# Kernel optimization log

Measured on AMD Instinct MI355X. Metric: run time of the kernel, lower is better.

## Reference

```python
import jax, jax.numpy as jnp
import numpy as np

BATCH = 8192
IN_F = 4096
OUT_F = 4096


def setup_inputs() -> dict:
    key = jax.random.key(0)
    k_x, k_w, k_m = jax.random.split(key, 3)
    x = jax.random.normal(k_x, (BATCH, IN_F), dtype=jnp.float32)
    # kaiming_normal_ for relu: std = sqrt(2 / fan_in) with fan_in = in_features
    std = float(np.sqrt(2.0 / IN_F))
    weight = jax.random.normal(k_w, (OUT_F, IN_F), dtype=jnp.float32) * std
    bias = jnp.zeros((OUT_F,), dtype=jnp.float32)
    mask = jax.random.bernoulli(k_m, 0.5, (OUT_F, IN_F)).astype(jnp.float32)
    return {"x": x, "weight": weight, "bias": bias, "mask": mask}


def reference(x, weight, bias, mask):
    # masked_weight = weight * mask; out = x @ masked_weight.T + bias
    masked_weight = weight * mask                      # [out, in]
    return jnp.einsum("bi,oi->bo", x, masked_weight) + bias  # [batch, out]
```

## Files before the change

kernel.cpp:

```cpp
#include <hip/hip_runtime.h>
#include <stdint.h>

#define BATCH 8192
#define IN_F  4096
#define OUT_F 4096

#define BM 256
#define BN 256
#define BK 64
#define KT (IN_F / BK)

typedef __attribute__((ext_vector_type(8))) short bf16x8;
typedef __attribute__((ext_vector_type(4))) float f32x4;


__device__ __forceinline__ unsigned short f2bf(float f) {
    unsigned int u = __float_as_uint(f);
    unsigned int lsb = (u >> 16) & 1u;
    u += 0x7fffu + lsb;
    return (unsigned short)(u >> 16);
}

__device__ __forceinline__ void gl_lds16(const void* g, void* l) {
    __builtin_amdgcn_global_load_lds(
        (const __attribute__((address_space(1))) void*)g,
        (__attribute__((address_space(3))) void*)l,
        16, 0, 0);
}

#define XF4 (BATCH * IN_F / 4)
#define WF4 (OUT_F * IN_F / 4)

__global__ __launch_bounds__(256) void cvt_kernel(const float4* __restrict__ x,
                                                  const float4* __restrict__ w,
                                                  const float4* __restrict__ m,
                                                  uint2* __restrict__ xo,
                                                  uint2* __restrict__ wo) {
    const int i = blockIdx.x * 256 + threadIdx.x;
    union { unsigned short u[4]; uint2 v; } r;
    if (i < XF4) {
        const float4 a = x[i];
        r.u[0] = f2bf(a.x); r.u[1] = f2bf(a.y);
        r.u[2] = f2bf(a.z); r.u[3] = f2bf(a.w);
        xo[i] = r.v;
    } else {
        const int j = i - XF4;
        const float4 a = w[j];
        const float4 b = m[j];
        r.u[0] = f2bf(a.x * b.x); r.u[1] = f2bf(a.y * b.y);
        r.u[2] = f2bf(a.z * b.z); r.u[3] = f2bf(a.w * b.w);
        wo[j] = r.v;
    }
}

__global__ __launch_bounds__(512, 2) void gemm_kernel(const unsigned short* __restrict__ A,
                                                      const unsigned short* __restrict__ W,
                                                      const float* __restrict__ bias,
                                                      float* __restrict__ C) {
    __shared__ __align__(16) char smem[131072];
    char* sA = smem;
    char* sB = smem + 65536;

    const int tid  = threadIdx.x;
    const int lane = tid & 63;
    const int wave = tid >> 6;
    const int wm   = wave >> 2;
    const int wn   = wave & 3;

    const int wg = ((blockIdx.x & 7) << 6) | (blockIdx.x >> 3);
    const int bm = wg >> 4;
    const int bn = wg & 15;

    const int r15 = lane & 15;
    const int g   = lane >> 4;
    const int k0  = (g ^ (r15 & 7)) << 4;

    int ldso[4];
    const unsigned short* gAp[4];
    const unsigned short* gBp[4];
#pragma unroll
    for (int i = 0; i < 4; ++i) {
        const int s   = i * 512 + tid;
        const int row = s >> 3;
        const int ch  = (s & 7) ^ (row & 7);
        ldso[i] = s * 16;
        gAp[i] = A + (size_t)(bm * BM + row) * IN_F + ch * 8;
        gBp[i] = W + (size_t)(bn * BN + row) * IN_F + ch * 8;
    }

#define GLA(buf, ktn, sl) gl_lds16(gAp[sl] + (ktn) * BK, sA + (buf) * 32768 + ldso[sl])
#define GLB(buf, ktn, sl) gl_lds16(gBp[sl] + (ktn) * BK, sB + (buf) * 32768 + ldso[sl])

    f32x4 acc[8][4] = {};
    bf16x8 af[2][2], bgf[4][2];

#define RDA(p)                                                               \
    do {                                                                     \
        _Pragma("unroll")                                                    \
        for (int i = 0; i < 2; ++i)                                          \
            _Pragma("unroll")                                                \
            for (int ks = 0; ks < 2; ++ks)                                   \
                af[i][ks] = *(const bf16x8*)(aB2 + ((p) * 2 + i) * 2048 +    \
                                             (k0 ^ (ks << 6)));              \
    } while (0)
#define RDB()                                                                \
    do {                                                                     \
        _Pragma("unroll")                                                    \
        for (int nf = 0; nf < 4; ++nf)                                       \
            _Pragma("unroll")                                                \
            for (int ks = 0; ks < 2; ++ks)                                   \
                bgf[nf][ks] = *(const bf16x8*)(bB2 + nf * 2048 +             \
                                               (k0 ^ (ks << 6)));            \
    } while (0)
#define MM(p)                                                                \
    do {                                                                     \
        __builtin_amdgcn_s_setprio(1);                                       \
        _Pragma("unroll")                                                    \
        for (int ks = 0; ks < 2; ++ks)                                       \
            _Pragma("unroll")                                                \
            for (int i = 0; i < 2; ++i)                                      \
                _Pragma("unroll")                                            \
                for (int nf = 0; nf < 4; ++nf)                               \
                    acc[(p) * 2 + i][nf] =                                   \
                        __builtin_amdgcn_mfma_f32_16x16x32_bf16(             \
                            af[i][ks], bgf[nf][ks], acc[(p) * 2 + i][nf],    \
                            0, 0, 0);                                        \
        __builtin_amdgcn_s_setprio(0);                                       \
    } while (0)
#define LG0   asm volatile("s_waitcnt lgkmcnt(0)" ::: "memory")
#define SBAR  __builtin_amdgcn_s_barrier()
#define SCH0  __builtin_amdgcn_sched_barrier(0)

    GLB(0, 0, 0); GLB(0, 0, 1); GLB(0, 0, 2); GLB(0, 0, 3);
    GLA(0, 0, 0); GLA(0, 0, 2); GLA(0, 0, 1); GLA(0, 0, 3);
    asm volatile("s_waitcnt vmcnt(2)" ::: "memory");
    SBAR; SCH0;

#pragma unroll 1
    for (int kt = 0; kt < KT; ++kt) {
        const int buf  = kt & 1;
        const int nb   = buf ^ 1;
        const bool more = (kt + 1 < KT);
        const char* aB2 = sA + buf * 32768 + ((wm * 128 + r15) << 7);
        const char* bB2 = sB + buf * 32768 + ((wn * 64 + r15) << 7);

        RDB(); RDA(0);
        if (more) { GLB(nb, kt + 1, 0); GLB(nb, kt + 1, 1); }
        asm volatile("s_waitcnt lgkmcnt(8)" ::: "memory");
        SBAR; LG0; SCH0;
        MM(0);
        SCH0; SBAR; SCH0;

        RDA(1);
        if (more) { GLB(nb, kt + 1, 2); GLB(nb, kt + 1, 3); }
        SBAR; LG0; SCH0;
        MM(1);
        SCH0;
        if (more) { asm volatile("s_waitcnt vmcnt(4)" ::: "memory"); }
        else      { asm volatile("s_waitcnt vmcnt(0)" ::: "memory"); }
        SBAR; SCH0;

        RDA(2);
        if (more) { GLA(nb, kt + 1, 0); GLA(nb, kt + 1, 2); }
        SBAR; LG0; SCH0;
        MM(2);
        SCH0; SBAR; SCH0;

        RDA(3);
        if (more) { GLA(nb, kt + 1, 1); GLA(nb, kt + 1, 3); }
        SBAR; LG0; SCH0;
        MM(3);
        SCH0;
        if (more) { asm volatile("s_waitcnt vmcnt(2)" ::: "memory"); }
        SBAR; SCH0;
    }
#undef GLA
#undef GLB
#undef RDA
#undef RDB
#undef MM
#undef LG0
#undef SBAR
#undef SCH0

    const int crow0 = bm * BM + wm * 128 + g * 4;
    const int ccol0 = bn * BN + wn * 64 + r15;
#pragma unroll
    for (int nf = 0; nf < 4; ++nf) {
        const int col = ccol0 + nf * 16;
        const float bj = bias[col];
#pragma unroll
        for (int mf = 0; mf < 8; ++mf)
#pragma unroll
            for (int reg = 0; reg < 4; ++reg) {
                const int row = crow0 + mf * 16 + reg;
                C[(size_t)row * OUT_F + col] = acc[mf][nf][reg] + bj;
            }
    }
}

__global__ __launch_bounds__(256) void fallback_kernel(const float* __restrict__ x,
                                                       const float* __restrict__ w,
                                                       const float* __restrict__ bias,
                                                       const float* __restrict__ m,
                                                       float* __restrict__ out) {
    size_t idx = (size_t)blockIdx.x * 256 + threadIdx.x;
    int row = (int)(idx >> 12);
    int col = (int)(idx & (OUT_F - 1));
    const float4* xr = (const float4*)(x + (size_t)row * IN_F);
    const float4* wr = (const float4*)(w + (size_t)col * IN_F);
    const float4* mr = (const float4*)(m + (size_t)col * IN_F);
    float s = 0.f;
    for (int k = 0; k < IN_F / 4; ++k) {
        float4 xv = xr[k], wv = wr[k], mv = mr[k];
        s += xv.x * wv.x * mv.x + xv.y * wv.y * mv.y +
             xv.z * wv.z * mv.z + xv.w * wv.w * mv.w;
    }
    out[idx] = s + bias[col];
}


extern "C" void kernel_launch(void* const* d_in, const int* in_sizes, int n_in,
                              void* d_out, int out_size, void* d_ws, size_t ws_size,
                              hipStream_t stream) {
    const float* x    = (const float*)d_in[0];
    const float* w    = (const float*)d_in[1];
    const float* bias = (const float*)d_in[2];
    const float* mask = (const float*)d_in[3];
    float* out = (float*)d_out;

    const size_t need = ((size_t)BATCH * IN_F + (size_t)OUT_F * IN_F) * sizeof(unsigned short);
    if (ws_size < need) {
        fallback_kernel<<<(size_t)BATCH * OUT_F / 256, 256, 0, stream>>>(
            x, w, bias, mask, out);
        return;
    }

    unsigned short* xb = (unsigned short*)d_ws;
    unsigned short* wb = xb + (size_t)BATCH * IN_F;

    cvt_kernel<<<(XF4 + WF4) / 256, 256, 0, stream>>>(
        (const float4*)x, (const float4*)w, (const float4*)mask,
        (uint2*)xb, (uint2*)wb);

    gemm_kernel<<<512, 512, 0, stream>>>(xb, wb, bias, out);
}
```

Measured before the change: 541.2 us.

## Triple-buffer B tiles and register-double-buffer A fragments to cut barriers

```diff
diff --git a/kernel.cpp b/kernel.cpp
--- a/kernel.cpp
+++ b/kernel.cpp
@@ -57,7 +57,7 @@
                                                       const unsigned short* __restrict__ W,
                                                       const float* __restrict__ bias,
                                                       float* __restrict__ C) {
-    __shared__ __align__(16) char smem[131072];
+    __shared__ __align__(16) char smem[163840];
     char* sA = smem;
     char* sB = smem + 65536;
 
@@ -77,7 +77,6 @@
 
     int ldso[4];
     const unsigned short* gAp[4];
-    const unsigned short* gBp[4];
 #pragma unroll
     for (int i = 0; i < 4; ++i) {
         const int s   = i * 512 + tid;
@@ -85,34 +84,37 @@
         const int ch  = (s & 7) ^ (row & 7);
         ldso[i] = s * 16;
         gAp[i] = A + (size_t)(bm * BM + row) * IN_F + ch * 8;
-        gBp[i] = W + (size_t)(bn * BN + row) * IN_F + ch * 8;
-    }
-
-#define GLA(buf, ktn, sl) gl_lds16(gAp[sl] + (ktn) * BK, sA + (buf) * 32768 + ldso[sl])
-#define GLB(buf, ktn, sl) gl_lds16(gBp[sl] + (ktn) * BK, sB + (buf) * 32768 + ldso[sl])
+    }
+    const ptrdiff_t bdel = (W + (size_t)bn * BN * IN_F) - (A + (size_t)bm * BM * IN_F);
+
+#define GLA(aoffb, ktn, sl) gl_lds16(gAp[sl] + (ktn) * BK, sA + (aoffb) + ldso[sl])
+#define GLB(boffb, ktn, sl) gl_lds16(gAp[sl] + bdel + (ktn) * BK, sB + (boffb) + ldso[sl])
+
+    const int arow = (wm * 128 + r15) << 7;
+    const int brow = (wn * 64 + r15) << 7;
 
     f32x4 acc[8][4] = {};
-    bf16x8 af[2][2], bgf[4][2];
-
-#define RDA(p)                                                               \
+    bf16x8 afA[2][2], afB[2][2], bgf[4][2];
+
+#define RDA(q, DST, abase)                                                   \
     do {                                                                     \
         _Pragma("unroll")                                                    \
         for (int i = 0; i < 2; ++i)                                          \
             _Pragma("unroll")                                                \
             for (int ks = 0; ks < 2; ++ks)                                   \
-                af[i][ks] = *(const bf16x8*)(aB2 + ((p) * 2 + i) * 2048 +    \
-                                             (k0 ^ (ks << 6)));              \
+                DST[i][ks] = *(const bf16x8*)((abase) +                      \
+                    (((q) * 32 + i * 16) << 7) + (k0 ^ (ks << 6)));          \
     } while (0)
-#define RDB()                                                                \
+#define RDB(bbase)                                                           \
     do {                                                                     \
         _Pragma("unroll")                                                    \
         for (int nf = 0; nf < 4; ++nf)                                       \
             _Pragma("unroll")                                                \
             for (int ks = 0; ks < 2; ++ks)                                   \
-                bgf[nf][ks] = *(const bf16x8*)(bB2 + nf * 2048 +             \
+                bgf[nf][ks] = *(const bf16x8*)((bbase) + nf * 2048 +         \
                                                (k0 ^ (ks << 6)));            \
     } while (0)
-#define MM(p)                                                                \
+#define MM(p, AX)                                                            \
     do {                                                                     \
         __builtin_amdgcn_s_setprio(1);                                       \
         _Pragma("unroll")                                                    \
@@ -123,63 +125,76 @@
                 for (int nf = 0; nf < 4; ++nf)                               \
                     acc[(p) * 2 + i][nf] =                                   \
                         __builtin_amdgcn_mfma_f32_16x16x32_bf16(             \
-                            af[i][ks], bgf[nf][ks], acc[(p) * 2 + i][nf],    \
+                            AX[i][ks], bgf[nf][ks], acc[(p) * 2 + i][nf],    \
                             0, 0, 0);                                        \
         __builtin_amdgcn_s_setprio(0);                                       \
     } while (0)
-#define LG0   asm volatile("s_waitcnt lgkmcnt(0)" ::: "memory")
+#define LGKM4 asm volatile("s_waitcnt lgkmcnt(4)" ::: "memory")
+#define LGKM0 asm volatile("s_waitcnt lgkmcnt(0)" ::: "memory")
 #define SBAR  __builtin_amdgcn_s_barrier()
 #define SCH0  __builtin_amdgcn_sched_barrier(0)
 
+    GLA(0, 0, 0); GLA(0, 0, 1); GLA(0, 0, 2); GLA(0, 0, 3);
     GLB(0, 0, 0); GLB(0, 0, 1); GLB(0, 0, 2); GLB(0, 0, 3);
-    GLA(0, 0, 0); GLA(0, 0, 2); GLA(0, 0, 1); GLA(0, 0, 3);
-    asm volatile("s_waitcnt vmcnt(2)" ::: "memory");
+    GLB(32768, 1, 0); GLB(32768, 1, 1); GLB(32768, 1, 2); GLB(32768, 1, 3);
+    asm volatile("s_waitcnt vmcnt(4)" ::: "memory");
     SBAR; SCH0;
+
+    RDB(sB + brow);
+    RDA(0, afA, sA + arow);
+    SCH0;
+
+    int bb1 = 32768;
+    int bb2 = 65536;
 
 #pragma unroll 1
     for (int kt = 0; kt < KT; ++kt) {
-        const int buf  = kt & 1;
-        const int nb   = buf ^ 1;
-        const bool more = (kt + 1 < KT);
-        const char* aB2 = sA + buf * 32768 + ((wm * 128 + r15) << 7);
-        const char* bB2 = sB + buf * 32768 + ((wn * 64 + r15) << 7);
-
-        RDB(); RDA(0);
-        if (more) { GLB(nb, kt + 1, 0); GLB(nb, kt + 1, 1); }
-        asm volatile("s_waitcnt lgkmcnt(8)" ::: "memory");
-        SBAR; LG0; SCH0;
-        MM(0);
-        SCH0; SBAR; SCH0;
-
-        RDA(1);
-        if (more) { GLB(nb, kt + 1, 2); GLB(nb, kt + 1, 3); }
-        SBAR; LG0; SCH0;
-        MM(1);
-        SCH0;
-        if (more) { asm volatile("s_waitcnt vmcnt(4)" ::: "memory"); }
-        else      { asm volatile("s_waitcnt vmcnt(0)" ::: "memory"); }
-        SBAR; SCH0;
-
-        RDA(2);
-        if (more) { GLA(nb, kt + 1, 0); GLA(nb, kt + 1, 2); }
-        SBAR; LG0; SCH0;
-        MM(2);
-        SCH0; SBAR; SCH0;
-
-        RDA(3);
-        if (more) { GLA(nb, kt + 1, 1); GLA(nb, kt + 1, 3); }
-        SBAR; LG0; SCH0;
-        MM(3);
-        SCH0;
-        if (more) { asm volatile("s_waitcnt vmcnt(2)" ::: "memory"); }
-        SBAR; SCH0;
+        const bool m1 = (kt + 1 < KT);
+        const bool m2 = (kt + 2 < KT);
+        const int  ab  = (kt & 1) << 15;
+        const int  abn = ab ^ 32768;
+        const char* aB  = sA + ab + arow;
+        const char* aBn = sA + abn + arow;
+
+        RDA(1, afB, aB);
+        if (m1) { GLA(abn, kt + 1, 0); GLA(abn, kt + 1, 2); }
+        SCH0; LGKM4; SCH0;
+        MM(0, afA);
+        SCH0;
+
+        RDA(2, afA, aB);
+        if (m1) { GLA(abn, kt + 1, 1); GLA(abn, kt + 1, 3); }
+        SCH0; LGKM4; SCH0;
+        MM(1, afB);
+        SCH0;
+
+        RDA(3, afB, aB);
+        if (m2) { GLB(bb2, kt + 2, 0); GLB(bb2, kt + 2, 1);
+                  GLB(bb2, kt + 2, 2); GLB(bb2, kt + 2, 3); }
+        SCH0; LGKM4; SCH0;
+        MM(2, afA);
+        SCH0; LGKM0; SCH0;
+        if (m2)      { asm volatile("s_waitcnt vmcnt(4)" ::: "memory"); SBAR; }
+        else if (m1) { asm volatile("s_waitcnt vmcnt(0)" ::: "memory"); SBAR; }
+        SCH0;
+
+        MM(3, afB);
+        if (m1) {
+            RDB(sB + bb1 + brow);
+            RDA(0, afA, aBn);
+        }
+        SCH0;
+
+        bb1 = bb2;
+        bb2 += 32768; if (bb2 == 98304) bb2 = 0;
     }
 #undef GLA
 #undef GLB
 #undef RDA
 #undef RDB
 #undef MM
-#undef LG0
+#undef LGKM4
+#undef LGKM0
 #undef SBAR
 #undef SCH0
 
```

Result: no change. 539.3 us (-0.3%).
